# Optimization experiments

Hardware: AMD Instinct MI355X
Metric: run time of the kernel (lower is better)

## Reference

```python
import jax, jax.numpy as jnp
import numpy as np

H = 64  # hidden_size

def _lstm_layer(x_tbd, W_ih, W_hh, b_ih, b_hh):
    """x_tbd: [T, B, D] -> outputs [T, B, H]. PyTorch gate order i,f,g,o."""
    T, B, _ = x_tbd.shape
    # input contribution precomputed for all timesteps: [T, B, 4H]
    xg = jnp.einsum('tbd,gd->tbg', x_tbd, W_ih) + b_ih + b_hh

    def step(carry, xg_t):
        h, c = carry
        gates = xg_t + h @ W_hh.T  # [B, 4H]
        i, f, g, o = jnp.split(gates, 4, axis=-1)
        i = jax.nn.sigmoid(i)
        f = jax.nn.sigmoid(f)
        g = jnp.tanh(g)
        o = jax.nn.sigmoid(o)
        c = f * c + i * g
        h = o * jnp.tanh(c)
        return (h, c), h

    h0 = jnp.zeros((B, H), dtype=x_tbd.dtype)
    c0 = jnp.zeros((B, H), dtype=x_tbd.dtype)
    _, hs = jax.lax.scan(step, (h0, c0), xg)
    return hs  # [T, B, H]


def setup_inputs() -> dict:
    key = jax.random.key(0)
    ks = jax.random.split(key, 16)
    B, T, D = 1024, 512, 32
    s = 1.0 / np.sqrt(H)  # PyTorch LSTM init scale
    return {
        'x': jax.random.normal(ks[0], (B, T, D), dtype=jnp.float32),
        'W_ih_l0': jax.random.uniform(ks[1], (4 * H, D), jnp.float32, -s, s),
        'W_hh_l0': jax.random.uniform(ks[2], (4 * H, H), jnp.float32, -s, s),
        'b_ih_l0': jax.random.uniform(ks[3], (4 * H,), jnp.float32, -s, s),
        'b_hh_l0': jax.random.uniform(ks[4], (4 * H,), jnp.float32, -s, s),
        'W_ih_l1': jax.random.uniform(ks[5], (4 * H, H), jnp.float32, -s, s),
        'W_hh_l1': jax.random.uniform(ks[6], (4 * H, H), jnp.float32, -s, s),
        'b_ih_l1': jax.random.uniform(ks[7], (4 * H,), jnp.float32, -s, s),
        'b_hh_l1': jax.random.uniform(ks[8], (4 * H,), jnp.float32, -s, s),
        'fc1_w': jax.random.uniform(ks[9], (H // 2, H), jnp.float32, -s, s),
        'fc1_b': jax.random.uniform(ks[10], (H // 2,), jnp.float32, -s, s),
        'fc2_w': jax.random.uniform(ks[11], (1, H // 2), jnp.float32, -0.25, 0.25),
        'fc2_b': jax.random.uniform(ks[12], (1,), jnp.float32, -0.25, 0.25),
    }


def reference(x, W_ih_l0, W_hh_l0, b_ih_l0, b_hh_l0,
              W_ih_l1, W_hh_l1, b_ih_l1, b_hh_l1,
              fc1_w, fc1_b, fc2_w, fc2_b):
    x_tbd = jnp.transpose(x, (1, 0, 2))  # [T, B, D]
    h1 = _lstm_layer(x_tbd, W_ih_l0, W_hh_l0, b_ih_l0, b_hh_l0)   # [T, B, H]
    h2 = _lstm_layer(h1,   W_ih_l1, W_hh_l1, b_ih_l1, b_hh_l1)   # [T, B, H]
    last = h2[-1]                       # [B, H] == lstm_out[:, -1, :]
    out = jax.nn.relu(last @ fc1_w.T + fc1_b)  # dropout is identity at eval
    out = out @ fc2_w.T + fc2_b         # [B, 1]
    return out
```

## Files before the change

### kernel.cpp

```cpp
#include <hip/hip_runtime.h>
#include <math.h>
#include <stdint.h>


namespace {

constexpr int Hh = 64, Dd = 32, Tt = 512, DEP = 6;
constexpr float LOG2E = 1.4426950408889634f;

typedef _Float16 f16x8 __attribute__((ext_vector_type(8)));
typedef float f32x4 __attribute__((ext_vector_type(4)));

__device__ __forceinline__ f32x4 mfma(f16x8 a, f16x8 b, f32x4 c) {
    return __builtin_amdgcn_mfma_f32_16x16x32_f16(a, b, c, 0, 0, 0);
}
__device__ __forceinline__ float rcpf(float x) { return __builtin_amdgcn_rcpf(x); }
__device__ __forceinline__ float exp2f_(float x) { return __builtin_amdgcn_exp2f(x); }
__device__ __forceinline__ float sigm_s(float p) { return rcpf(1.0f + exp2f_(-p)); }
__device__ __forceinline__ float tanh_s(float p) {
    return 1.0f - 2.0f * rcpf(exp2f_(p) + 1.0f);
}
__device__ __forceinline__ float tanh_n(float c) {
    return 1.0f - 2.0f * rcpf(exp2f_(c * (2.0f * LOG2E)) + 1.0f);
}
__device__ __forceinline__ f16x8 cvt8s(const float* p, float sc) {
    f16x8 r;
#pragma unroll
    for (int e = 0; e < 8; ++e) r[e] = (_Float16)(p[e] * sc);
    return r;
}
__device__ __forceinline__ int ld_acq(const int* p) {
    return __hip_atomic_load(p, __ATOMIC_ACQUIRE, __HIP_MEMORY_SCOPE_WORKGROUP);
}
__device__ __forceinline__ void add_rel(int* p, int v) {
    __hip_atomic_fetch_add(p, v, __ATOMIC_RELEASE, __HIP_MEMORY_SCOPE_WORKGROUP);
}

__global__ __launch_bounds__(512, 2) void lstm_f16(
    const float* __restrict__ x,
    const float* __restrict__ Wih0,
    const float* __restrict__ Whh0,
    const float* __restrict__ bih0, const float* __restrict__ bhh0,
    const float* __restrict__ Wih1,
    const float* __restrict__ Whh1,
    const float* __restrict__ bih1, const float* __restrict__ bhh1,
    const float* __restrict__ fc1w,
    const float* __restrict__ fc1b,
    const float* __restrict__ fc2w,
    const float* __restrict__ fc2b,
    float* __restrict__ out)
{
    __shared__ __align__(16) _Float16 s_h0[DEP][2][16][8];
    __shared__ __align__(16) _Float16 s_h1[DEP][2][16][8];
    __shared__ int s_cnt0[DEP];
    __shared__ int s_cnt1[DEP];
    __shared__ int s_cons;
    __shared__ float s_hf[Hh][5];
    __shared__ float s_fcw[32 * 65];
    __shared__ float s_fc[32][5];

    const int tid = threadIdx.x;
    const int w = tid >> 6;
    const int l = tid & 63;
    const int ar = l & 15;
    const int akb = l >> 4;
    const int cq = l >> 4;
    const int cj = l & 15;
    const int cb = cj & 3;
    const int dd = cj >> 2;
    const bool isL1w = (w >= 4);
    const int wl = w & 3;
    const int b0 = blockIdx.x * 4;

    const int r4 = ar & 3;
    const float sc = (r4 == 2) ? 2.0f * LOG2E : LOG2E;
    const int grow = r4 * 64 + 16 * wl + 4 * (ar >> 2);
    f16x8 Afr[4][4];
    if (!isL1w) {
#pragma unroll
        for (int i = 0; i < 4; ++i) {
            const int g = grow + i;
            Afr[i][0] = cvt8s(Wih0 + g * Dd + akb * 8, sc);
            Afr[i][1] = cvt8s(Whh0 + g * Hh + akb * 8, sc);
            Afr[i][2] = cvt8s(Whh0 + g * Hh + 32 + akb * 8, sc);
            Afr[i][3] = Afr[i][1];
        }
    } else {
#pragma unroll
        for (int i = 0; i < 4; ++i) {
            const int g = grow + i;
            Afr[i][0] = cvt8s(Wih1 + g * Hh + akb * 8, sc);
            Afr[i][1] = cvt8s(Wih1 + g * Hh + 32 + akb * 8, sc);
            Afr[i][2] = cvt8s(Whh1 + g * Hh + akb * 8, sc);
            Afr[i][3] = cvt8s(Whh1 + g * Hh + 32 + akb * 8, sc);
        }
    }

    const float* bi = isL1w ? bih1 : bih0;
    const float* bhp = isL1w ? bhh1 : bhh0;
    f32x4 biasT[4];
#pragma unroll
    for (int i = 0; i < 4; ++i)
#pragma unroll
        for (int r = 0; r < 4; ++r) {
            const float s2 = (r == 2) ? 2.0f * LOG2E : LOG2E;
            const int uu = 16 * wl + 4 * cq + i;
            biasT[i][r] = s2 * (bi[r * 64 + uu] + bhp[r * 64 + uu]);
        }

    const int ub = 16 * wl + 4 * cq + dd;
    const int kf_h = ub >> 5;
    const int row_h = ((ub & 31) >> 3) * 4 + cb;
    const int e_h = ub & 7;
    _Float16* const wb0 = &s_h0[0][kf_h][row_h][e_h];
    _Float16* const wb1 = &s_h1[0][kf_h][row_h][e_h];

    const int rrow = (l >> 4) * 4 + (l & 3);
    const _Float16* const rb0 = &s_h0[0][0][rrow][0];
    const _Float16* const rb1 = &s_h1[0][0][rrow][0];

    {
        int* p0 = (int*)s_h0;
        int* p1 = (int*)s_h1;
        for (int i = tid; i < DEP * 128; i += 512) { p0[i] = 0; p1[i] = 0; }
        if (tid < DEP) {
            s_cnt0[tid] = (tid == 0) ? 4 : 0;
            s_cnt1[tid] = (tid == 0) ? 4 : 0;
        }
        if (tid == DEP) s_cons = 0;
    }
    __syncthreads();

    float lasth = 0.f;

    if (!isL1w) {
        const float* xbase = x + ((size_t)(b0 + cb) * Tt) * Dd + akb * 8;
        float4 xr0 = *(const float4*)(xbase);
        float4 xr1 = *(const float4*)(xbase + 4);
        f16x8 xcur;
#pragma unroll
        for (int e = 0; e < 4; ++e) {
            xcur[e] = (_Float16)xr0[e];
            xcur[4 + e] = (_Float16)xr1[e];
        }
        xr0 = *(const float4*)(xbase + Dd);
        xr1 = *(const float4*)(xbase + Dd + 4);

        float cst = 0.f;
        int rs = 0, tgt = 4;
        for (int t = 0; t < Tt; ++t) {
            while (ld_acq(&s_cnt0[rs]) < tgt) __builtin_amdgcn_s_sleep(1);
            const f16x8 b0a = *(const f16x8*)(rb0 + rs * 256);
            const f16x8 b0b = *(const f16x8*)(rb0 + rs * 256 + 128);

            f32x4 acc[4];
#pragma unroll
            for (int i = 0; i < 4; ++i) {
                f32x4 a = mfma(Afr[i][0], xcur, biasT[i]);
                a = mfma(Afr[i][1], b0a, a);
                a = mfma(Afr[i][2], b0b, a);
                acc[i] = a;
            }
            f16x8 xn;
#pragma unroll
            for (int e = 0; e < 4; ++e) {
                xn[e] = (_Float16)xr0[e];
                xn[4 + e] = (_Float16)xr1[e];
            }
            const int tf = (t + 2 < Tt) ? (t + 2) : (Tt - 1);
            xr0 = *(const float4*)(xbase + (size_t)tf * Dd);
            xr1 = *(const float4*)(xbase + (size_t)tf * Dd + 4);
            xcur = xn;

            const f32x4 g01 = (dd & 1) ? acc[1] : acc[0];
            const f32x4 g23 = (dd & 1) ? acc[3] : acc[2];
            const f32x4 gg = (dd & 2) ? g23 : g01;
            const float gi = sigm_s(gg[0]);
            const float gf = sigm_s(gg[1]);
            const float zz = tanh_s(gg[2]);
            const float go = sigm_s(gg[3]);
            cst = gf * cst + gi * zz;
            const float hv = go * tanh_n(cst);

            const int ws = (rs + 1 == DEP) ? 0 : rs + 1;
            if (t >= DEP - 1)
                while (ld_acq(&s_cons) < 4 * (t - 4)) __builtin_amdgcn_s_sleep(1);
            wb0[ws * 256] = (_Float16)hv;
            if (l == 0) add_rel(&s_cnt0[ws], 1);
            rs = ws;
            if (rs == 0) tgt += 4;
        }
    } else {
        float cst = 0.f;
        int rs0 = 1, t0 = 4;
        int rs1 = 0, t1 = 4;
        for (int s = 0; s < Tt; ++s) {
            while (ld_acq(&s_cnt0[rs0]) < t0) __builtin_amdgcn_s_sleep(1);
            while (ld_acq(&s_cnt1[rs1]) < t1) __builtin_amdgcn_s_sleep(1);
            const f16x8 b0a = *(const f16x8*)(rb0 + rs0 * 256);
            const f16x8 b0b = *(const f16x8*)(rb0 + rs0 * 256 + 128);
            const f16x8 b1a = *(const f16x8*)(rb1 + rs1 * 256);
            const f16x8 b1b = *(const f16x8*)(rb1 + rs1 * 256 + 128);

            f32x4 acc[4];
#pragma unroll
            for (int i = 0; i < 4; ++i) {
                f32x4 a = mfma(Afr[i][0], b0a, biasT[i]);
                a = mfma(Afr[i][1], b0b, a);
                a = mfma(Afr[i][2], b1a, a);
                a = mfma(Afr[i][3], b1b, a);
                acc[i] = a;
            }
            const f32x4 g01 = (dd & 1) ? acc[1] : acc[0];
            const f32x4 g23 = (dd & 1) ? acc[3] : acc[2];
            const f32x4 gg = (dd & 2) ? g23 : g01;
            const float gi = sigm_s(gg[0]);
            const float gf = sigm_s(gg[1]);
            const float zz = tanh_s(gg[2]);
            const float go = sigm_s(gg[3]);
            cst = gf * cst + gi * zz;
            const float hv = go * tanh_n(cst);
            lasth = hv;

            wb1[rs0 * 256] = (_Float16)hv;
            if (l == 0) {
                add_rel(&s_cnt1[rs0], 1);
                add_rel(&s_cons, 1);
            }
            rs1 = rs0;
            t1 = t0;
            rs0 = (rs0 + 1 == DEP) ? 0 : rs0 + 1;
            if (rs0 == 0) t0 += 4;
        }
        s_hf[ub][cb] = lasth;
    }
    __syncthreads();

    for (int i2 = tid; i2 < 32 * 64; i2 += 512) {
        const int m = i2 >> 6, uu = i2 & 63;
        s_fcw[m * 65 + uu] = fc1w[i2];
    }
    __syncthreads();
    if (tid < 128) {
        const int m = tid >> 2, jj = tid & 3;
        float acc = fc1b[m];
#pragma unroll
        for (int uu = 0; uu < Hh; ++uu)
            acc = fmaf(s_fcw[m * 65 + uu], s_hf[uu][jj], acc);
        s_fc[m][jj] = fmaxf(acc, 0.f);
    }
    __syncthreads();
    if (tid < 4) {
        float acc = fc2b[0];
#pragma unroll
        for (int m = 0; m < 32; ++m)
            acc = fmaf(fc2w[m], s_fc[m][tid], acc);
        out[b0 + tid] = acc;
    }
}

}

extern "C" void kernel_launch(void* const* d_in, const int* in_sizes, int n_in,
                              void* d_out, int out_size, void* d_ws, size_t ws_size,
                              hipStream_t stream) {
    const float* x    = (const float*)d_in[0];
    const float* Wih0 = (const float*)d_in[1];
    const float* Whh0 = (const float*)d_in[2];
    const float* bih0 = (const float*)d_in[3];
    const float* bhh0 = (const float*)d_in[4];
    const float* Wih1 = (const float*)d_in[5];
    const float* Whh1 = (const float*)d_in[6];
    const float* bih1 = (const float*)d_in[7];
    const float* bhh1 = (const float*)d_in[8];
    const float* fc1w = (const float*)d_in[9];
    const float* fc1b = (const float*)d_in[10];
    const float* fc2w = (const float*)d_in[11];
    const float* fc2b = (const float*)d_in[12];
    float* out = (float*)d_out;

    lstm_f16<<<dim3(256), dim3(512), 0, stream>>>(
        x, Wih0, Whh0, bih0, bhh0, Wih1, Whh1, bih1, bhh1,
        fc1w, fc1b, fc2w, fc2b, out);
}
```

Before: 271.7 us.

## Replace atomic counters with per-wave flags and precompute off-critical-path gate partials

Swaps the LDS atomic acquire/release counters for per-wave 16-bit sequence flags, polled with volatile loads and ordered with explicit lgkmcnt waits. It also moves the x-input MFMA (layer 0) and the layer-0 h input MFMAs (layer 1) off the recurrent critical path, so each step only runs the recurrent MFMAs after its wait. The ring depth grows to 8 so slot indices are bit masks. Relying on volatile LDS polling and s_waitcnt instead of atomics trades synchronization cost for subtle memory-ordering risk and busy spinning without sleep.

Measured after the change: 385.0 us. 41.7% more time.

```diff
diff --git a/kernel.cpp b/kernel.cpp
--- a/kernel.cpp
+++ b/kernel.cpp
@@ -5,7 +5,7 @@
 
 namespace {
 
-constexpr int Hh = 64, Dd = 32, Tt = 512, DEP = 6;
+constexpr int Hh = 64, Dd = 32, Tt = 512, DEP = 8;
 constexpr float LOG2E = 1.4426950408889634f;
 
 typedef _Float16 f16x8 __attribute__((ext_vector_type(8)));
@@ -29,11 +29,19 @@
     for (int e = 0; e < 8; ++e) r[e] = (_Float16)(p[e] * sc);
     return r;
 }
-__device__ __forceinline__ int ld_acq(const int* p) {
-    return __hip_atomic_load(p, __ATOMIC_ACQUIRE, __HIP_MEMORY_SCOPE_WORKGROUP);
-}
-__device__ __forceinline__ void add_rel(int* p, int v) {
-    __hip_atomic_fetch_add(p, v, __ATOMIC_RELEASE, __HIP_MEMORY_SCOPE_WORKGROUP);
+__device__ __forceinline__ uint32_t umin_(uint32_t a, uint32_t b) {
+    return a < b ? a : b;
+}
+__device__ __forceinline__ int min4u(uint32_t a, uint32_t b) {
+    return (int)umin_(umin_(a & 0xffffu, a >> 16), umin_(b & 0xffffu, b >> 16));
+}
+__device__ __forceinline__ void pollflags(const unsigned short* f, int tgt) {
+    const volatile uint32_t* p = (const volatile uint32_t*)f;
+    for (;;) {
+        const uint32_t a = p[0], b = p[1];
+        if (min4u(a, b) >= tgt) break;
+    }
+    asm volatile("" ::: "memory");
 }
 
 __global__ __launch_bounds__(512, 2) void lstm_f16(
@@ -52,9 +60,9 @@
 {
     __shared__ __align__(16) _Float16 s_h0[DEP][2][16][8];
     __shared__ __align__(16) _Float16 s_h1[DEP][2][16][8];
-    __shared__ int s_cnt0[DEP];
-    __shared__ int s_cnt1[DEP];
-    __shared__ int s_cons;
+    __shared__ __align__(8) unsigned short s_f0[DEP][4];
+    __shared__ __align__(8) unsigned short s_f1[DEP][4];
+    __shared__ __align__(8) unsigned short s_pr1[4];
     __shared__ float s_hf[Hh][5];
     __shared__ float s_fcw[32 * 65];
     __shared__ float s_fc[32][5];
@@ -112,8 +120,8 @@
     const int kf_h = ub >> 5;
     const int row_h = ((ub & 31) >> 3) * 4 + cb;
     const int e_h = ub & 7;
-    _Float16* const wb0 = &s_h0[0][kf_h][row_h][e_h];
-    _Float16* const wb1 = &s_h1[0][kf_h][row_h][e_h];
+    _Float16* const wb = isL1w ? &s_h1[0][kf_h][row_h][e_h]
+                               : &s_h0[0][kf_h][row_h][e_h];
 
     const int rrow = (l >> 4) * 4 + (l & 3);
     const _Float16* const rb0 = &s_h0[0][0][rrow][0];
@@ -123,55 +131,43 @@
         int* p0 = (int*)s_h0;
         int* p1 = (int*)s_h1;
         for (int i = tid; i < DEP * 128; i += 512) { p0[i] = 0; p1[i] = 0; }
-        if (tid < DEP) {
-            s_cnt0[tid] = (tid == 0) ? 4 : 0;
-            s_cnt1[tid] = (tid == 0) ? 4 : 0;
-        }
-        if (tid == DEP) s_cons = 0;
+        if (tid < DEP * 2) ((int*)s_f0)[tid] = 0;
+        if (tid < 2) ((int*)s_pr1)[tid] = 0;
     }
     __syncthreads();
-
-    float lasth = 0.f;
 
     if (!isL1w) {
         const float* xbase = x + ((size_t)(b0 + cb) * Tt) * Dd + akb * 8;
-        float4 xr0 = *(const float4*)(xbase);
-        float4 xr1 = *(const float4*)(xbase + 4);
+        float4 xra = *(const float4*)(xbase);
+        float4 xrb = *(const float4*)(xbase + 4);
         f16x8 xcur;
 #pragma unroll
         for (int e = 0; e < 4; ++e) {
-            xcur[e] = (_Float16)xr0[e];
-            xcur[4 + e] = (_Float16)xr1[e];
-        }
-        xr0 = *(const float4*)(xbase + Dd);
-        xr1 = *(const float4*)(xbase + Dd + 4);
+            xcur[e] = (_Float16)xra[e];
+            xcur[4 + e] = (_Float16)xrb[e];
+        }
+        xra = *(const float4*)(xbase + Dd);
+        xrb = *(const float4*)(xbase + Dd + 4);
+
+        f32x4 xpart[4];
+#pragma unroll
+        for (int i = 0; i < 4; ++i) xpart[i] = mfma(Afr[i][0], xcur, biasT[i]);
 
         float cst = 0.f;
-        int rs = 0, tgt = 4;
         for (int t = 0; t < Tt; ++t) {
-            while (ld_acq(&s_cnt0[rs]) < tgt) __builtin_amdgcn_s_sleep(1);
+            const int rs = t & 7, ws = (t + 1) & 7;
+            pollflags(&s_f0[rs][0], t);
             const f16x8 b0a = *(const f16x8*)(rb0 + rs * 256);
             const f16x8 b0b = *(const f16x8*)(rb0 + rs * 256 + 128);
+            const volatile uint32_t* bp = (const volatile uint32_t*)&s_pr1[0];
+            const uint32_t bpa = bp[0], bpb = bp[1];
 
             f32x4 acc[4];
 #pragma unroll
             for (int i = 0; i < 4; ++i) {
-                f32x4 a = mfma(Afr[i][0], xcur, biasT[i]);
-                a = mfma(Afr[i][1], b0a, a);
-                a = mfma(Afr[i][2], b0b, a);
-                acc[i] = a;
-            }
-            f16x8 xn;
-#pragma unroll
-            for (int e = 0; e < 4; ++e) {
-                xn[e] = (_Float16)xr0[e];
-                xn[4 + e] = (_Float16)xr1[e];
-            }
-            const int tf = (t + 2 < Tt) ? (t + 2) : (Tt - 1);
-            xr0 = *(const float4*)(xbase + (size_t)tf * Dd);
-            xr1 = *(const float4*)(xbase + (size_t)tf * Dd + 4);
-            xcur = xn;
-
+                f32x4 a = mfma(Afr[i][1], b0a, xpart[i]);
+                acc[i] = mfma(Afr[i][2], b0b, a);
+            }
             const f32x4 g01 = (dd & 1) ? acc[1] : acc[0];
             const f32x4 g23 = (dd & 1) ? acc[3] : acc[2];
             const f32x4 gg = (dd & 2) ? g23 : g01;
@@ -182,34 +178,47 @@
             cst = gf * cst + gi * zz;
             const float hv = go * tanh_n(cst);
 
-            const int ws = (rs + 1 == DEP) ? 0 : rs + 1;
-            if (t >= DEP - 1)
-                while (ld_acq(&s_cons) < 4 * (t - 4)) __builtin_amdgcn_s_sleep(1);
-            wb0[ws * 256] = (_Float16)hv;
-            if (l == 0) add_rel(&s_cnt0[ws], 1);
-            rs = ws;
-            if (rs == 0) tgt += 4;
+            if (min4u(bpa, bpb) < t - 7) pollflags(&s_pr1[0], t - 7);
+            wb[ws * 256] = (_Float16)hv;
+            asm volatile("s_waitcnt lgkmcnt(0)" ::: "memory");
+            if (l == 0) s_f0[ws][wl] = (unsigned short)(t + 1);
+
+            f16x8 xn;
+#pragma unroll
+            for (int e = 0; e < 4; ++e) {
+                xn[e] = (_Float16)xra[e];
+                xn[4 + e] = (_Float16)xrb[e];
+            }
+            const int tf = (t + 2 < Tt) ? (t + 2) : (Tt - 1);
+            xra = *(const float4*)(xbase + (size_t)tf * Dd);
+            xrb = *(const float4*)(xbase + (size_t)tf * Dd + 4);
+            xcur = xn;
+#pragma unroll
+            for (int i = 0; i < 4; ++i) xpart[i] = mfma(Afr[i][0], xcur, biasT[i]);
         }
     } else {
-        float cst = 0.f;
-        int rs0 = 1, t0 = 4;
-        int rs1 = 0, t1 = 4;
+        f32x4 part[4];
+        {
+            pollflags(&s_f0[1][0], 1);
+            const f16x8 a0 = *(const f16x8*)(rb0 + 1 * 256);
+            const f16x8 a1 = *(const f16x8*)(rb0 + 1 * 256 + 128);
+#pragma unroll
+            for (int i = 0; i < 4; ++i) {
+                f32x4 p = mfma(Afr[i][0], a0, biasT[i]);
+                part[i] = mfma(Afr[i][1], a1, p);
+            }
+        }
+        float cst = 0.f, lasth = 0.f;
         for (int s = 0; s < Tt; ++s) {
-            while (ld_acq(&s_cnt0[rs0]) < t0) __builtin_amdgcn_s_sleep(1);
-            while (ld_acq(&s_cnt1[rs1]) < t1) __builtin_amdgcn_s_sleep(1);
-            const f16x8 b0a = *(const f16x8*)(rb0 + rs0 * 256);
-            const f16x8 b0b = *(const f16x8*)(rb0 + rs0 * 256 + 128);
-            const f16x8 b1a = *(const f16x8*)(rb1 + rs1 * 256);
-            const f16x8 b1b = *(const f16x8*)(rb1 + rs1 * 256 + 128);
-
+            const int rs = s & 7, ws = (s + 1) & 7;
+            pollflags(&s_f1[rs][0], s);
+            const f16x8 b1a = *(const f16x8*)(rb1 + rs * 256);
+            const f16x8 b1b = *(const f16x8*)(rb1 + rs * 256 + 128);
             f32x4 acc[4];
 #pragma unroll
             for (int i = 0; i < 4; ++i) {
-                f32x4 a = mfma(Afr[i][0], b0a, biasT[i]);
-                a = mfma(Afr[i][1], b0b, a);
-                a = mfma(Afr[i][2], b1a, a);
-                a = mfma(Afr[i][3], b1b, a);
-                acc[i] = a;
+                f32x4 a = mfma(Afr[i][2], b1a, part[i]);
+                acc[i] = mfma(Afr[i][3], b1b, a);
             }
             const f32x4 g01 = (dd & 1) ? acc[1] : acc[0];
             const f32x4 g23 = (dd & 1) ? acc[3] : acc[2];
@@ -222,15 +231,23 @@
             const float hv = go * tanh_n(cst);
             lasth = hv;
 
-            wb1[rs0 * 256] = (_Float16)hv;
-            if (l == 0) {
-                add_rel(&s_cnt1[rs0], 1);
-                add_rel(&s_cons, 1);
-            }
-            rs1 = rs0;
-            t1 = t0;
-            rs0 = (rs0 + 1 == DEP) ? 0 : rs0 + 1;
-            if (rs0 == 0) t0 += 4;
+            wb[ws * 256] = (_Float16)hv;
+            asm volatile("s_waitcnt lgkmcnt(0)" ::: "memory");
+            if (l == 0) s_f1[ws][wl] = (unsigned short)(s + 1);
+
+            if (s + 1 < Tt) {
+                const int r0 = (s + 2) & 7;
+                pollflags(&s_f0[r0][0], s + 2);
+                const f16x8 a0 = *(const f16x8*)(rb0 + r0 * 256);
+                const f16x8 a1 = *(const f16x8*)(rb0 + r0 * 256 + 128);
+#pragma unroll
+                for (int i = 0; i < 4; ++i) {
+                    f32x4 p = mfma(Afr[i][0], a0, biasT[i]);
+                    part[i] = mfma(Afr[i][1], a1, p);
+                }
+                asm volatile("s_waitcnt lgkmcnt(0)" ::: "memory");
+                if (l == 0) s_pr1[wl] = (unsigned short)(s + 1);
+            }
         }
         s_hf[ub][cb] = lasth;
     }
```
